# Kernel optimization log

Hardware: AMD Instinct MI355X
Metric: run time of the kernel (lower is better)

Reference implementation:

```python
import jax, jax.numpy as jnp
import numpy as np

N, E, D, L, G, T = 50000, 600000, 128, 4, 512, 10
EPS = 1e-5


def setup_inputs() -> dict:
    key = jax.random.key(0)
    ks = jax.random.split(key, 20)
    s = lambda k, shp, fan: jax.random.normal(k, shp, jnp.float32) * (1.0 / np.sqrt(fan))
    inp = {
        'x': jax.random.normal(ks[0], (N, 3), jnp.float32),
        'edge_index': jax.random.randint(ks[1], (2, E), 0, N, jnp.int32),
        'batch': jnp.sort(jax.random.randint(ks[2], (N,), 0, G, jnp.int32)),
        'emb_W': s(ks[3], (3, D), 3),
        'emb_b': jnp.zeros((D,), jnp.float32),
        'conv_W': s(ks[4], (L, 12 * D, D), 12 * D),
        'conv_b': jnp.zeros((L, D), jnp.float32),
        'bn_gamma': jnp.ones((L, D), jnp.float32),
        'bn_beta': jnp.zeros((L, D), jnp.float32),
        'W1': s(ks[5], (D, D // 2), D), 'b1': jnp.zeros((D // 2,), jnp.float32),
        'W2': s(ks[6], (D // 2, D // 4), D // 2), 'b2': jnp.zeros((D // 4,), jnp.float32),
        'W3': s(ks[7], (D // 4, T), D // 4), 'b3': jnp.zeros((T,), jnp.float32),
    }
    return inp


def reference(x, edge_index, batch, emb_W, emb_b, conv_W, conv_b, bn_gamma, bn_beta,
              W1, b1, W2, b2, W3, b3):
    n = x.shape[0]
    src, dst = edge_index[0], edge_index[1]  # messages flow src(j) -> dst(i)
    deg = jax.ops.segment_sum(jnp.ones((src.shape[0],), x.dtype), dst, num_segments=n)
    delta = jnp.mean(jnp.log1p(deg))          # avg log-degree (PNA's avg_deg['log'])
    d = jnp.maximum(deg, 1.0)[:, None]        # clamp(min=1)
    log_d = jnp.log1p(d)
    amp, att = log_d / delta, delta / log_d   # amplification / attenuation scalers
    has_edge = (deg > 0)[:, None]

    h = x @ emb_W + emb_b                     # node_emb Linear(3, D)
    for l in range(conv_W.shape[0]):
        msg = h[src]                          # [E, D] gather
        s1 = jax.ops.segment_sum(msg, dst, num_segments=n)
        s2 = jax.ops.segment_sum(msg * msg, dst, num_segments=n)
        mean = s1 / d
        std = jnp.sqrt(jax.nn.relu(s2 / d - mean * mean) + EPS)
        mn = jnp.where(has_edge, jax.ops.segment_min(msg, dst, num_segments=n), 0.0)
        mx = jnp.where(has_edge, jax.ops.segment_max(msg, dst, num_segments=n), 0.0)
        aggs = jnp.concatenate([mean, mn, mx, std], axis=-1)                 # [N, 4D]
        out = jnp.concatenate([aggs, aggs * amp, aggs * att], axis=-1)       # [N, 12D]
        out = out @ conv_W[l] + conv_b[l]      # post_nn Linear(12D, D)
        mu = out.mean(axis=0)
        var = out.var(axis=0)
        out = (out - mu) * jax.lax.rsqrt(var + EPS) * bn_gamma[l] + bn_beta[l]
        h = jax.nn.relu(out) + h               # residual (dropout off: eval)

    # global_mean_pool over graphs
    gsum = jax.ops.segment_sum(h, batch, num_segments=G)
    cnt = jnp.maximum(jax.ops.segment_sum(jnp.ones((n,), h.dtype), batch, num_segments=G), 1.0)
    g = gsum / cnt[:, None]
    g = jax.nn.relu(g @ W1 + b1)
    g = jax.nn.relu(g @ W2 + b2)
    return g @ W3 + b3                         # source='image': no clamp
```

## Files before the change

kernel.cpp:

```cpp
#include <hip/hip_runtime.h>
#include <math.h>

#define NN 50000
#define NE 600000
#define DD 128
#define NL 4
#define NG 512
#define NT 10
#define NPAD 50176
#define EPSF 1e-5f

typedef __bf16 bf16x8 __attribute__((ext_vector_type(8)));
typedef float f32x4 __attribute__((ext_vector_type(4)));

__device__ __forceinline__ unsigned short f2bf(float x) {
    union { float f; unsigned u; } v; v.f = x;
    unsigned r = v.u + 0x7FFFu + ((v.u >> 16) & 1u);
    return (unsigned short)(r >> 16);
}
__device__ __forceinline__ unsigned pack_bf2(float a, float b) {
    return (unsigned)f2bf(a) | ((unsigned)f2bf(b) << 16);
}
__device__ __forceinline__ float bf_lo(unsigned v) {
    union { unsigned u; float f; } w; w.u = (v & 0xFFFFu) << 16; return w.f;
}
__device__ __forceinline__ float bf_hi(unsigned v) {
    union { unsigned u; float f; } w; w.u = v & 0xFFFF0000u; return w.f;
}

__global__ void k_count(const int* __restrict__ dst, int* __restrict__ deg,
                        float* __restrict__ dsum, int E) {
    int e = blockIdx.x * blockDim.x + threadIdx.x;
    if (e == 0) *dsum = 0.f;
    if (e < E) atomicAdd(&deg[dst[e]], 1);
}

__global__ void k_scan_part(const int* __restrict__ deg, int* __restrict__ part,
                            float* __restrict__ dsum, int n) {
    __shared__ int sm[256];
    int b = blockIdx.x, t = threadIdx.x;
    int base = b * 1024 + t * 4;
    int s = 0;
    float ls = 0.f;
    #pragma unroll
    for (int j = 0; j < 4; j++)
        if (base + j < n) { int d = deg[base + j]; s += d; ls += log1pf((float)d); }
    sm[t] = s;
    #pragma unroll
    for (int off = 32; off > 0; off >>= 1) ls += __shfl_down(ls, off);
    if ((t & 63) == 0) atomicAdd(dsum, ls);
    __syncthreads();
    for (int off = 128; off > 0; off >>= 1) {
        if (t < off) sm[t] += sm[t + off];
        __syncthreads();
    }
    if (t == 0) part[b] = sm[0];
}

__global__ void k_scan_top(const int* __restrict__ part, int* __restrict__ offs,
                           int* __restrict__ row_ptr, int nb, int n) {
    __shared__ int sm[64];
    int t = threadIdx.x;
    int v = (t < nb) ? part[t] : 0;
    sm[t] = v;
    __syncthreads();
    #pragma unroll
    for (int off = 1; off < 64; off <<= 1) {
        int y = (t >= off) ? sm[t - off] : 0;
        __syncthreads();
        sm[t] += y;
        __syncthreads();
    }
    if (t < nb) offs[t] = sm[t] - v;
    if (t == nb - 1) row_ptr[n] = sm[t];
}

__global__ void k_scan_apply(const int* __restrict__ deg, const int* __restrict__ offs,
                             int* __restrict__ row_ptr, int* __restrict__ cursor, int n) {
    __shared__ int sm[256];
    int b = blockIdx.x, t = threadIdx.x;
    int base = b * 1024 + t * 4;
    int v[4]; int s = 0;
    #pragma unroll
    for (int j = 0; j < 4; j++) { v[j] = (base + j < n) ? deg[base + j] : 0; s += v[j]; }
    sm[t] = s;
    __syncthreads();
    for (int off = 1; off < 256; off <<= 1) {
        int y = (t >= off) ? sm[t - off] : 0;
        __syncthreads();
        sm[t] += y;
        __syncthreads();
    }
    int run = offs[b] + sm[t] - s;
    #pragma unroll
    for (int j = 0; j < 4; j++) {
        if (base + j < n) { row_ptr[base + j] = run; cursor[base + j] = run; run += v[j]; }
    }
}

__global__ void k_fill(const int* __restrict__ src, const int* __restrict__ dst,
                       int* __restrict__ cursor, int* __restrict__ csr_src, int E) {
    int e = blockIdx.x * blockDim.x + threadIdx.x;
    if (e < E) {
        int d = dst[e];
        int pos = atomicAdd(&cursor[d], 1);
        csr_src[pos] = src[e];
    }
}

__global__ void k_scalars(const int* __restrict__ deg, const float* __restrict__ dsum,
                          float* __restrict__ inv_d, float* __restrict__ amp,
                          float* __restrict__ att, int n) {
    int i = blockIdx.x * blockDim.x + threadIdx.x;
    if (i >= n) return;
    float delta = *dsum / (float)n;
    float d = fmaxf((float)deg[i], 1.f);
    float ld = log1pf(d);
    inv_d[i] = 1.f / d;
    amp[i] = ld / delta;
    att[i] = delta / ld;
}

__global__ void k_emb(const float* __restrict__ x, const float* __restrict__ W,
                      const float* __restrict__ b, unsigned* __restrict__ hb2, int total2) {
    int i = blockIdx.x * blockDim.x + threadIdx.x;
    if (i >= total2) return;
    int node = i >> 6, c = (i & 63) * 2;
    float x0 = x[node * 3 + 0], x1 = x[node * 3 + 1], x2 = x[node * 3 + 2];
    float v0 = x0 * W[c] + x1 * W[DD + c] + x2 * W[2 * DD + c] + b[c];
    float v1 = x0 * W[c + 1] + x1 * W[DD + c + 1] + x2 * W[2 * DD + c + 1] + b[c + 1];
    hb2[i] = pack_bf2(v0, v1);
}

__global__ void k_wconv(const float* __restrict__ W, unsigned short* __restrict__ Bt2, int total) {
    int o = blockIdx.x * blockDim.x + threadIdx.x;
    if (o >= total) return;
    int l = o / 196608;
    int idx = o % 196608;
    int kc = idx / 3072;
    int rem = idx % 3072;
    int j = rem >> 10;
    int nn = (rem >> 3) & 127;
    int k8 = rem & 7;
    int k = kc * 8 + k8;
    Bt2[o] = f2bf(W[(size_t)l * 196608 + (size_t)(j * 512 + k) * 128 + nn]);
}

__global__ void k_agg(const unsigned* __restrict__ hb2, const int* __restrict__ row_ptr,
                      const int* __restrict__ csr_src, const float* __restrict__ inv_d,
                      unsigned* __restrict__ atw, float* __restrict__ bn_zero) {
    __shared__ unsigned ldsb[16 * 260];
    int tid = threadIdx.x;
    if (blockIdx.x == 0) bn_zero[tid] = 0.f;
    int w = tid >> 6, t = tid & 63;
    int node0 = blockIdx.x * 16;

    #pragma unroll 1
    for (int pp = 0; pp < 2; pp++) {
        int nlA = w * 4 + pp * 2;
        int nodeA = node0 + nlA, nodeB = nodeA + 1;
        int bgA = row_ptr[nodeA], enA = row_ptr[nodeA + 1];
        int bgB = row_ptr[nodeB], enB = row_ptr[nodeB + 1];
        float s1[2][2] = {{0.f,0.f},{0.f,0.f}};
        float s2[2][2] = {{0.f,0.f},{0.f,0.f}};
        float mn[2][2] = {{INFINITY,INFINITY},{INFINITY,INFINITY}};
        float mx[2][2] = {{-INFINITY,-INFINITY},{-INFINITY,-INFINITY}};
        auto ACC = [&](int ns, unsigned v) {
            float a = bf_lo(v), b = bf_hi(v);
            s1[ns][0] += a; s2[ns][0] += a * a;
            mn[ns][0] = fminf(mn[ns][0], a); mx[ns][0] = fmaxf(mx[ns][0], a);
            s1[ns][1] += b; s2[ns][1] += b * b;
            mn[ns][1] = fminf(mn[ns][1], b); mx[ns][1] = fmaxf(mx[ns][1], b);
        };
        int ea = bgA, eb = bgB;
        while (ea + 3 < enA && eb + 3 < enB) {
            int ia0 = csr_src[ea],     ia1 = csr_src[ea + 1];
            int ia2 = csr_src[ea + 2], ia3 = csr_src[ea + 3];
            int ib0 = csr_src[eb],     ib1 = csr_src[eb + 1];
            int ib2 = csr_src[eb + 2], ib3 = csr_src[eb + 3];
            unsigned va0 = hb2[(size_t)ia0 * 64 + t];
            unsigned va1 = hb2[(size_t)ia1 * 64 + t];
            unsigned va2 = hb2[(size_t)ia2 * 64 + t];
            unsigned va3 = hb2[(size_t)ia3 * 64 + t];
            unsigned vb0 = hb2[(size_t)ib0 * 64 + t];
            unsigned vb1 = hb2[(size_t)ib1 * 64 + t];
            unsigned vb2 = hb2[(size_t)ib2 * 64 + t];
            unsigned vb3 = hb2[(size_t)ib3 * 64 + t];
            ACC(0, va0); ACC(0, va1); ACC(0, va2); ACC(0, va3);
            ACC(1, vb0); ACC(1, vb1); ACC(1, vb2); ACC(1, vb3);
            ea += 4; eb += 4;
        }
        for (; ea + 3 < enA; ea += 4) {
            int i0 = csr_src[ea], i1 = csr_src[ea + 1];
            int i2 = csr_src[ea + 2], i3 = csr_src[ea + 3];
            unsigned v0 = hb2[(size_t)i0 * 64 + t];
            unsigned v1 = hb2[(size_t)i1 * 64 + t];
            unsigned v2 = hb2[(size_t)i2 * 64 + t];
            unsigned v3 = hb2[(size_t)i3 * 64 + t];
            ACC(0, v0); ACC(0, v1); ACC(0, v2); ACC(0, v3);
        }
        for (; ea < enA; ea++) ACC(0, hb2[(size_t)csr_src[ea] * 64 + t]);
        for (; eb + 3 < enB; eb += 4) {
            int i0 = csr_src[eb], i1 = csr_src[eb + 1];
            int i2 = csr_src[eb + 2], i3 = csr_src[eb + 3];
            unsigned v0 = hb2[(size_t)i0 * 64 + t];
            unsigned v1 = hb2[(size_t)i1 * 64 + t];
            unsigned v2 = hb2[(size_t)i2 * 64 + t];
            unsigned v3 = hb2[(size_t)i3 * 64 + t];
            ACC(1, v0); ACC(1, v1); ACC(1, v2); ACC(1, v3);
        }
        for (; eb < enB; eb++) ACC(1, hb2[(size_t)csr_src[eb] * 64 + t]);

        #pragma unroll
        for (int ns = 0; ns < 2; ns++) {
            int node = (ns == 0) ? nodeA : nodeB;
            int nl = nlA + ns;
            int bg = (ns == 0) ? bgA : bgB;
            int en = (ns == 0) ? enA : enB;
            float id = inv_d[node];
            float meana = s1[ns][0] * id, meanb = s1[ns][1] * id;
            float sda = sqrtf(fmaxf(s2[ns][0] * id - meana * meana, 0.f) + EPSF);
            float sdb = sqrtf(fmaxf(s2[ns][1] * id - meanb * meanb, 0.f) + EPSF);
            float mna = mn[ns][0], mnb = mn[ns][1];
            float mxa = mx[ns][0], mxb = mx[ns][1];
            if (bg == en) { mna = 0.f; mxa = 0.f; mnb = 0.f; mxb = 0.f; }
            int base = nl * 260;
            ldsb[base + 0 * 64 + t] = pack_bf2(meana, meanb);
            ldsb[base + 1 * 64 + t] = pack_bf2(mna, mnb);
            ldsb[base + 2 * 64 + t] = pack_bf2(mxa, mxb);
            ldsb[base + 3 * 64 + t] = pack_bf2(sda, sdb);
        }
    }
    __syncthreads();
    #pragma unroll
    for (int p = 0; p < 4; p++) {
        int id = p * 256 + tid;
        int node = id & 15, c = id >> 4;
        int sec = c >> 4, cb = c & 15;
        const unsigned* s = &ldsb[node * 260 + sec * 64 + cb * 4];
        uint4 v = make_uint4(s[0], s[1], s[2], s[3]);
        *(uint4*)&atw[((size_t)c * NPAD + node0 + node) * 4] = v;
    }
}

__global__ __launch_bounds__(256, 2) void k_gemm_mfma(
    const unsigned short* __restrict__ At, const unsigned short* __restrict__ Bt2,
    const float* __restrict__ bias, const float* __restrict__ amp,
    const float* __restrict__ att, unsigned short* __restrict__ outb,
    float* __restrict__ bn_sum, float* __restrict__ bn_sq, int n) {
    int tid = threadIdx.x;
    int w = tid >> 6, lane = tid & 63;
    int quad = lane >> 4, l16 = lane & 15;
    int bid = blockIdx.x;
    int tile = (bid >> 5) * 8 + (bid & 7);
    int cg = (bid >> 3) & 3;
    if (tile >= 196) return;
    int c0 = cg * 32;
    int base = tile * 256 + w * 64;

    f32x4 acc[4][2][3];
    #pragma unroll
    for (int rt = 0; rt < 4; rt++)
        #pragma unroll
        for (int ct = 0; ct < 2; ct++)
            #pragma unroll
            for (int j = 0; j < 3; j++) acc[rt][ct][j] = (f32x4)(0.f);

    const unsigned short* pA = At + ((size_t)quad * NPAD + base + l16) * 8;
    const unsigned short* pB = Bt2 + ((size_t)quad * 384 + c0 + l16) * 8;
    const size_t stepA = (size_t)4 * NPAD * 8;
    const int stepB = 4 * 384 * 8;

    bf16x8 af0[4], af1[4], af2[4], bf0[2][3], bf1[2][3], bf2[2][3];
    auto loadA = [&](bf16x8* dst) {
        #pragma unroll
        for (int rt = 0; rt < 4; rt++) dst[rt] = *(const bf16x8*)(pA + rt * 128);
        pA += stepA;
    };
    auto loadB = [&](bf16x8 (*dst)[3]) {
        #pragma unroll
        for (int ct = 0; ct < 2; ct++)
            #pragma unroll
            for (int j = 0; j < 3; j++)
                dst[ct][j] = *(const bf16x8*)(pB + j * 1024 + ct * 128);
        pB += stepB;
    };
    auto domfma = [&](bf16x8* af, bf16x8 (*bf)[3]) {
        #pragma unroll
        for (int ct = 0; ct < 2; ct++)
            #pragma unroll
            for (int j = 0; j < 3; j++)
                #pragma unroll
                for (int rt = 0; rt < 4; rt++)
                    acc[rt][ct][j] = __builtin_amdgcn_mfma_f32_16x16x32_bf16(
                        af[rt], bf[ct][j], acc[rt][ct][j], 0, 0, 0);
    };

    loadA(af0); loadB(bf0);
    loadA(af1); loadB(bf1);
    #pragma unroll 1
    for (int it = 0; it < 15; it += 3) {
        loadA(af2); loadB(bf2);
        domfma(af0, bf0);
        loadA(af0); loadB(bf0);
        domfma(af1, bf1);
        loadA(af1); loadB(bf1);
        domfma(af2, bf2);
    }
    domfma(af0, bf0);

    float psum[2] = {0.f, 0.f}, psq[2] = {0.f, 0.f};
    #pragma unroll
    for (int rt = 0; rt < 4; rt++) {
        #pragma unroll
        for (int reg = 0; reg < 4; reg++) {
            int row = base + rt * 16 + quad * 4 + reg;
            if (row < n) {
                float am = amp[row], at = att[row];
                #pragma unroll
                for (int ct = 0; ct < 2; ct++) {
                    int col = c0 + ct * 16 + l16;
                    float v = acc[rt][ct][0][reg] + am * acc[rt][ct][1][reg]
                            + at * acc[rt][ct][2][reg] + bias[col];
                    outb[(size_t)row * DD + col] = f2bf(v);
                    psum[ct] += v;
                    psq[ct] += v * v;
                }
            }
        }
    }
    #pragma unroll
    for (int ct = 0; ct < 2; ct++) {
        psum[ct] += __shfl_xor(psum[ct], 16, 64);
        psum[ct] += __shfl_xor(psum[ct], 32, 64);
        psq[ct]  += __shfl_xor(psq[ct], 16, 64);
        psq[ct]  += __shfl_xor(psq[ct], 32, 64);
    }
    if (quad == 0) {
        #pragma unroll
        for (int ct = 0; ct < 2; ct++) {
            int col = c0 + ct * 16 + l16;
            atomicAdd(&bn_sum[col], psum[ct]);
            atomicAdd(&bn_sq[col], psq[ct]);
        }
    }
}

__global__ void k_bnapply(const unsigned* __restrict__ outb2, const float* __restrict__ bn_sum,
                          const float* __restrict__ bn_sq, const float* __restrict__ gamma,
                          const float* __restrict__ beta, unsigned* __restrict__ hb2,
                          int total8) {
    int i = blockIdx.x * blockDim.x + threadIdx.x;
    if (i >= total8) return;
    int c = (i & 15) * 8;
    const float invn = 1.f / (float)NN;
    uint4 ov = ((const uint4*)outb2)[i];
    uint4 hv = ((const uint4*)hb2)[i];
    unsigned ou[4] = {ov.x, ov.y, ov.z, ov.w};
    unsigned hu[4] = {hv.x, hv.y, hv.z, hv.w};
    unsigned ru[4];
    #pragma unroll
    for (int p = 0; p < 4; p++) {
        int c0 = c + p * 2;
        float mu0 = bn_sum[c0] * invn;
        float var0 = bn_sq[c0] * invn - mu0 * mu0;
        float sc0 = rsqrtf(var0 + EPSF) * gamma[c0];
        float sh0 = beta[c0] - mu0 * sc0;
        float mu1 = bn_sum[c0 + 1] * invn;
        float var1 = bn_sq[c0 + 1] * invn - mu1 * mu1;
        float sc1 = rsqrtf(var1 + EPSF) * gamma[c0 + 1];
        float sh1 = beta[c0 + 1] - mu1 * sc1;
        float v0 = fmaxf(bf_lo(ou[p]) * sc0 + sh0, 0.f) + bf_lo(hu[p]);
        float v1 = fmaxf(bf_hi(ou[p]) * sc1 + sh1, 0.f) + bf_hi(hu[p]);
        ru[p] = pack_bf2(v0, v1);
    }
    ((uint4*)hb2)[i] = make_uint4(ru[0], ru[1], ru[2], ru[3]);
}

__global__ void k_pool_mlp(const unsigned* __restrict__ hb2, const int* __restrict__ batch,
                           const float* __restrict__ W1, const float* __restrict__ b1,
                           const float* __restrict__ W2, const float* __restrict__ b2,
                           const float* __restrict__ W3, const float* __restrict__ b3,
                           float* __restrict__ out, int n) {
    __shared__ float gvec[128];
    __shared__ float h1[64];
    __shared__ float h2[32];
    __shared__ int srange[2];
    int g = blockIdx.x;
    int t = threadIdx.x;
    if (t < 2) {
        int target = g + t;
        int lo = 0, hi = n;
        while (lo < hi) {
            int mid = (lo + hi) >> 1;
            if (batch[mid] < target) lo = mid + 1; else hi = mid;
        }
        srange[t] = lo;
    }
    __syncthreads();
    int s = srange[0], e = srange[1];
    int p = t >> 1, odd = t & 1;
    float acc = 0.f;
    for (int i = s; i < e; i++) {
        unsigned v = hb2[(size_t)i * 64 + p];
        acc += odd ? bf_hi(v) : bf_lo(v);
    }
    float cnt = fmaxf((float)(e - s), 1.f);
    gvec[t] = acc / cnt;
    __syncthreads();
    if (t < 64) {
        float a = b1[t];
        for (int k = 0; k < 128; k++) a += gvec[k] * W1[k * 64 + t];
        h1[t] = fmaxf(a, 0.f);
    }
    __syncthreads();
    if (t < 32) {
        float a = b2[t];
        for (int k = 0; k < 64; k++) a += h1[k] * W2[k * 32 + t];
        h2[t] = fmaxf(a, 0.f);
    }
    __syncthreads();
    if (t < 10) {
        float a = b3[t];
        for (int k = 0; k < 32; k++) a += h2[k] * W3[k * 10 + t];
        out[g * NT + t] = a;
    }
}

extern "C" void kernel_launch(void* const* d_in, const int* in_sizes, int n_in,
                              void* d_out, int out_size, void* d_ws, size_t ws_size,
                              hipStream_t stream) {
    const float* x      = (const float*)d_in[0];
    const int*   eidx   = (const int*)d_in[1];
    const int*   batch  = (const int*)d_in[2];
    const float* emb_W  = (const float*)d_in[3];
    const float* emb_b  = (const float*)d_in[4];
    const float* conv_W = (const float*)d_in[5];
    const float* conv_b = (const float*)d_in[6];
    const float* bn_g   = (const float*)d_in[7];
    const float* bn_b   = (const float*)d_in[8];
    const float* W1 = (const float*)d_in[9];
    const float* b1 = (const float*)d_in[10];
    const float* W2 = (const float*)d_in[11];
    const float* b2 = (const float*)d_in[12];
    const float* W3 = (const float*)d_in[13];
    const float* b3 = (const float*)d_in[14];
    float* out = (float*)d_out;

    const int* src = eidx;
    const int* dst = eidx + NE;

    char* p = (char*)d_ws;
    auto carve = [&](size_t bytes) {
        void* r = (void*)p;
        p += (bytes + 255) & ~(size_t)255;
        return r;
    };
    int* deg      = (int*)carve(NN * 4);
    int* row_ptr  = (int*)carve((NN + 1) * 4);
    int* cursor   = (int*)carve(NN * 4);
    int* csr_src  = (int*)carve(NE * 4);
    int* part     = (int*)carve(64 * 4);
    int* offs     = (int*)carve(64 * 4);
    float* inv_d  = (float*)carve(NN * 4);
    float* amp    = (float*)carve(NN * 4);
    float* att    = (float*)carve(NN * 4);
    float* dsum   = (float*)carve(4);
    float* bn_sum = (float*)carve(DD * 4);
    float* bn_sq  = (float*)carve(DD * 4);
    unsigned* hb2 = (unsigned*)carve((size_t)NN * 64 * 4);
    unsigned* At  = (unsigned*)carve((size_t)68 * NPAD * 16);
    unsigned short* outb = (unsigned short*)carve((size_t)NN * DD * 2);
    unsigned short* Bt2 = (unsigned short*)carve(((size_t)NL * 196608 + 12288) * 2);

    hipMemsetAsync(deg, 0, NN * 4, stream);

    const int NSB = (NN + 1023) / 1024;
    k_count<<<(NE + 255) / 256, 256, 0, stream>>>(dst, deg, dsum, NE);
    k_scan_part<<<NSB, 256, 0, stream>>>(deg, part, dsum, NN);
    k_scan_top<<<1, 64, 0, stream>>>(part, offs, row_ptr, NSB, NN);
    k_scan_apply<<<NSB, 256, 0, stream>>>(deg, offs, row_ptr, cursor, NN);
    k_fill<<<(NE + 255) / 256, 256, 0, stream>>>(src, dst, cursor, csr_src, NE);
    k_scalars<<<(NN + 255) / 256, 256, 0, stream>>>(deg, dsum, inv_d, amp, att, NN);
    k_emb<<<(NN * 64 + 255) / 256, 256, 0, stream>>>(x, emb_W, emb_b, hb2, NN * 64);
    k_wconv<<<(NL * 196608 + 255) / 256, 256, 0, stream>>>(conv_W, Bt2, NL * 196608);

    const int gemm_blocks = 800;
    for (int l = 0; l < NL; l++) {
        k_agg<<<NN / 16, 256, 0, stream>>>(hb2, row_ptr, csr_src, inv_d, At, bn_sum);
        k_gemm_mfma<<<gemm_blocks, 256, 0, stream>>>(
            (const unsigned short*)At, Bt2 + (size_t)l * 196608,
            conv_b + l * DD, amp, att, outb, bn_sum, bn_sq, NN);
        k_bnapply<<<(NN * 16 + 255) / 256, 256, 0, stream>>>(
            (const unsigned*)outb, bn_sum, bn_sq, bn_g + l * DD, bn_b + l * DD, hb2, NN * 16);
    }

    k_pool_mlp<<<NG, 128, 0, stream>>>(hb2, batch, W1, b1, W2, b2, W3, b3, out, NN);
}
```

Before: 551.5 us.

## Interleave K-chunks in aggregation output layout and fold degree scalars into scan

```diff
diff --git a/kernel.cpp b/kernel.cpp
--- a/kernel.cpp
+++ b/kernel.cpp
@@ -76,7 +76,9 @@
 }
 
 __global__ void k_scan_apply(const int* __restrict__ deg, const int* __restrict__ offs,
-                             int* __restrict__ row_ptr, int* __restrict__ cursor, int n) {
+                             int* __restrict__ row_ptr, int* __restrict__ cursor,
+                             const float* __restrict__ dsum, float* __restrict__ inv_d,
+                             float* __restrict__ amp, float* __restrict__ att, int n) {
     __shared__ int sm[256];
     int b = blockIdx.x, t = threadIdx.x;
     int base = b * 1024 + t * 4;
@@ -92,9 +94,17 @@
         __syncthreads();
     }
     int run = offs[b] + sm[t] - s;
+    float delta = *dsum / (float)n;
     #pragma unroll
     for (int j = 0; j < 4; j++) {
-        if (base + j < n) { row_ptr[base + j] = run; cursor[base + j] = run; run += v[j]; }
+        if (base + j < n) {
+            row_ptr[base + j] = run; cursor[base + j] = run; run += v[j];
+            float d = fmaxf((float)v[j], 1.f);
+            float ld = log1pf(d);
+            inv_d[base + j] = 1.f / d;
+            amp[base + j] = ld / delta;
+            att[base + j] = delta / ld;
+        }
     }
 }
 
@@ -106,19 +116,6 @@
         int pos = atomicAdd(&cursor[d], 1);
         csr_src[pos] = src[e];
     }
-}
-
-__global__ void k_scalars(const int* __restrict__ deg, const float* __restrict__ dsum,
-                          float* __restrict__ inv_d, float* __restrict__ amp,
-                          float* __restrict__ att, int n) {
-    int i = blockIdx.x * blockDim.x + threadIdx.x;
-    if (i >= n) return;
-    float delta = *dsum / (float)n;
-    float d = fmaxf((float)deg[i], 1.f);
-    float ld = log1pf(d);
-    inv_d[i] = 1.f / d;
-    amp[i] = ld / delta;
-    att[i] = delta / ld;
 }
 
 __global__ void k_emb(const float* __restrict__ x, const float* __restrict__ W,
@@ -235,11 +232,14 @@
     #pragma unroll
     for (int p = 0; p < 4; p++) {
         int id = p * 256 + tid;
-        int node = id & 15, c = id >> 4;
-        int sec = c >> 4, cb = c & 15;
-        const unsigned* s = &ldsb[node * 260 + sec * 64 + cb * 4];
+        int q2 = id & 3;
+        int node = (id >> 2) & 15;
+        int kc4 = id >> 6;
+        int kc = kc4 * 4 + q2;
+        int sec = kc >> 4, cw = kc & 15;
+        const unsigned* s = &ldsb[node * 260 + sec * 64 + cw * 4];
         uint4 v = make_uint4(s[0], s[1], s[2], s[3]);
-        *(uint4*)&atw[((size_t)c * NPAD + node0 + node) * 4] = v;
+        *(uint4*)&atw[((size_t)kc4 * NPAD + node0 + node) * 16 + q2 * 4] = v;
     }
 }
 
@@ -266,15 +266,15 @@
             #pragma unroll
             for (int j = 0; j < 3; j++) acc[rt][ct][j] = (f32x4)(0.f);
 
-    const unsigned short* pA = At + ((size_t)quad * NPAD + base + l16) * 8;
+    const unsigned short* pA = At + (size_t)(base + l16) * 32 + quad * 8;
     const unsigned short* pB = Bt2 + ((size_t)quad * 384 + c0 + l16) * 8;
-    const size_t stepA = (size_t)4 * NPAD * 8;
+    const size_t stepA = (size_t)NPAD * 32;
     const int stepB = 4 * 384 * 8;
 
     bf16x8 af0[4], af1[4], af2[4], bf0[2][3], bf1[2][3], bf2[2][3];
     auto loadA = [&](bf16x8* dst) {
         #pragma unroll
-        for (int rt = 0; rt < 4; rt++) dst[rt] = *(const bf16x8*)(pA + rt * 128);
+        for (int rt = 0; rt < 4; rt++) dst[rt] = *(const bf16x8*)(pA + rt * 512);
         pA += stepA;
     };
     auto loadB = [&](bf16x8 (*dst)[3]) {
@@ -469,7 +469,7 @@
     float* bn_sum = (float*)carve(DD * 4);
     float* bn_sq  = (float*)carve(DD * 4);
     unsigned* hb2 = (unsigned*)carve((size_t)NN * 64 * 4);
-    unsigned* At  = (unsigned*)carve((size_t)68 * NPAD * 16);
+    unsigned* At  = (unsigned*)carve((size_t)18 * NPAD * 64);
     unsigned short* outb = (unsigned short*)carve((size_t)NN * DD * 2);
     unsigned short* Bt2 = (unsigned short*)carve(((size_t)NL * 196608 + 12288) * 2);
 
@@ -479,9 +479,9 @@
     k_count<<<(NE + 255) / 256, 256, 0, stream>>>(dst, deg, dsum, NE);
     k_scan_part<<<NSB, 256, 0, stream>>>(deg, part, dsum, NN);
     k_scan_top<<<1, 64, 0, stream>>>(part, offs, row_ptr, NSB, NN);
-    k_scan_apply<<<NSB, 256, 0, stream>>>(deg, offs, row_ptr, cursor, NN);
+    k_scan_apply<<<NSB, 256, 0, stream>>>(deg, offs, row_ptr, cursor, dsum,
+                                          inv_d, amp, att, NN);
     k_fill<<<(NE + 255) / 256, 256, 0, stream>>>(src, dst, cursor, csr_src, NE);
-    k_scalars<<<(NN + 255) / 256, 256, 0, stream>>>(deg, dsum, inv_d, amp, att, NN);
     k_emb<<<(NN * 64 + 255) / 256, 256, 0, stream>>>(x, emb_W, emb_b, hb2, NN * 64);
     k_wconv<<<(NL * 196608 + 255) / 256, 256, 0, stream>>>(conv_W, Bt2, NL * 196608);
 
```

Result: slower. 566.9 us (+2.8%).
